# Performance work log

Hardware: AMD Instinct MI355X
Metric: run time of the kernel (lower is better)

## Reference

```python
import jax, jax.numpy as jnp
import numpy as np
import math

RANK = 396

def setup_inputs() -> dict:
    key = jax.random.key(0)
    ks = jax.random.split(key, 8)
    batch, L, wemb, temb, tags, rank = 16, 128, 400, 20, 25, RANK
    std = 0.1545
    return {
        "word_emb": jax.random.normal(ks[0], (batch, L, wemb), dtype=jnp.float32),
        "tag_emd": jax.random.normal(ks[1], (tags, temb), dtype=jnp.float32),
        "W1": jax.random.normal(ks[2], (wemb, rank), dtype=jnp.float32) * std,
        "W2": jax.random.normal(ks[3], (wemb, rank), dtype=jnp.float32) * std,
        "W3": jax.random.normal(ks[4], (wemb, rank), dtype=jnp.float32) * std,
        "T1": jax.random.normal(ks[5], (temb, rank), dtype=jnp.float32) * std,
        "T2": jax.random.normal(ks[6], (temb, rank), dtype=jnp.float32) * std,
        "T3": jax.random.normal(ks[7], (temb, rank), dtype=jnp.float32) * std,
    }

def reference(word_emb, tag_emd, W1, W2, W3, T1, T2, T3):
    # word_emb: [n, L, wemb]; output: [n, L-2, tags, tags, tags]
    g1 = word_emb[:, :-2] @ W1   # [n, m, k]
    g2 = word_emb[:, 1:-1] @ W2
    g3 = word_emb[:, 2:] @ W3
    g4 = tag_emd @ T1            # [a, k]
    g5 = tag_emd @ T2
    g6 = tag_emd @ T3
    temp01 = g1 * g2 * g3                               # [n, m, k]
    temp02 = jnp.einsum('ak,bk,ck->abck', g4, g5, g6)   # [a, b, c, k]
    score = jnp.einsum('nmk,abck->nmabc', temp01, temp02)
    score = score / jnp.asarray(math.sqrt(RANK), score.dtype)
    return score
```

## Files before the change

kernel.cpp:

```cpp
#include <hip/hip_runtime.h>
#include <hip/hip_bf16.h>
#include <stdint.h>

#define KP    416
#define RANKD 396
#define WEMB  400
#define TEMB  20
#define TAGS  25
#define BATCH 16
#define LSEQ  128
#define MROWS 126
#define NM    2016
#define NMP   2048
#define ABC   15625
#define ABCP  15872
#define SCALE 0.050251890762960605f

typedef __attribute__((ext_vector_type(8))) short short8;
typedef __attribute__((ext_vector_type(4))) float f32x4;

#define OFF_T01  0
#define OFF_T02  1703936
#define OFF_WORD 14909440
#define OFF_WT   16613376
#define OFF_G    17651712

#define GLOAD_LDS16(gp, lp) \
  __builtin_amdgcn_global_load_lds((const __attribute__((address_space(1))) uint32_t*)(gp), \
                                   (__attribute__((address_space(3))) uint32_t*)(lp), 16, 0, 0)

__device__ __forceinline__ uint16_t f2bf(float f) {
    union { float f; uint32_t u; } v; v.f = f;
    uint32_t u = v.u;
    return (uint16_t)((u + 0x7FFFu + ((u >> 16) & 1u)) >> 16);
}

#define J1_BLK 3328
#define J2_BLK 2028
#define J3_BLK 122
__global__ void k_prep(const float* __restrict__ word,
                       const float* __restrict__ W1, const float* __restrict__ W2,
                       const float* __restrict__ W3, const float* __restrict__ tag,
                       const float* __restrict__ T1, const float* __restrict__ T2,
                       const float* __restrict__ T3,
                       uint16_t* __restrict__ wordb, uint16_t* __restrict__ wt,
                       float* __restrict__ g) {
    int bx = blockIdx.x;
    if (bx < J1_BLK) {
        int idx = bx * 256 + threadIdx.x;
        int e = idx % KP, row = idx / KP;
        wordb[idx] = f2bf((e < WEMB) ? word[row * WEMB + e] : 0.f);
    } else if (bx < J1_BLK + J2_BLK) {
        int idx = (bx - J1_BLK) * 256 + threadIdx.x;
        int j = idx / (KP * KP);
        int rem = idx % (KP * KP);
        int k = rem / KP, e = rem % KP;
        const float* W = (j == 0) ? W1 : (j == 1) ? W2 : W3;
        wt[idx] = f2bf((k < RANKD && e < WEMB) ? W[e * RANKD + k] : 0.f);
    } else {
        int idx = (bx - J1_BLK - J2_BLK) * 256 + threadIdx.x;
        if (idx >= 3 * TAGS * KP) return;
        int j = idx / (TAGS * KP);
        int rem = idx % (TAGS * KP);
        int a = rem / KP, k = rem % KP;
        const float* T = (j == 0) ? T1 : (j == 1) ? T2 : T3;
        float s = 0.f;
        if (k < RANKD) {
            for (int e = 0; e < TEMB; ++e) s += tag[a * TEMB + e] * T[e * RANKD + k];
        }
        g[idx] = s;
    }
}

#define T01_BLK 896
#define T02_BLK 3224
__global__ __launch_bounds__(256) void k_mid(const uint16_t* __restrict__ word,
                                             const uint16_t* __restrict__ wt,
                                             const float* __restrict__ g,
                                             uint16_t* __restrict__ t01,
                                             uint16_t* __restrict__ t02) {
    int bx = blockIdx.x;
    if (bx < T01_BLK) {
        int wid = threadIdx.x >> 6, lane = threadIdx.x & 63;
        int nmtile = bx & 127;
        int ktile = (bx >> 7) * 4 + wid;
        if (ktile >= KP / 16) return;
        int col_l = lane & 15, kblk = lane >> 4;
        int colk = ktile * 16 + col_l;
        f32x4 acc1 = {0.f, 0.f, 0.f, 0.f}, acc2 = acc1, acc3 = acc1;
        if (nmtile < NM / 16) {
            int nm_a = nmtile * 16 + col_l;
            int n = nm_a / MROWS, m = nm_a % MROWS;
            const uint16_t* arow = word + (size_t)(n * LSEQ + m) * KP;
            const uint16_t* b1 = wt + (size_t)colk * KP;
            const uint16_t* b2 = wt + (size_t)KP * KP + (size_t)colk * KP;
            const uint16_t* b3 = wt + (size_t)2 * KP * KP + (size_t)colk * KP;
            for (int e0 = 0; e0 < KP; e0 += 32) {
                int eo = e0 + kblk * 8;
                short8 a0 = *(const short8*)(arow + eo);
                short8 a1 = *(const short8*)(arow + KP + eo);
                short8 a2 = *(const short8*)(arow + 2 * KP + eo);
                short8 v1 = *(const short8*)(b1 + eo);
                short8 v2 = *(const short8*)(b2 + eo);
                short8 v3 = *(const short8*)(b3 + eo);
                acc1 = __builtin_amdgcn_mfma_f32_16x16x32_bf16(a0, v1, acc1, 0, 0, 0);
                acc2 = __builtin_amdgcn_mfma_f32_16x16x32_bf16(a1, v2, acc2, 0, 0, 0);
                acc3 = __builtin_amdgcn_mfma_f32_16x16x32_bf16(a2, v3, acc3, 0, 0, 0);
            }
        }
        for (int r = 0; r < 4; ++r) {
            int row = nmtile * 16 + kblk * 4 + r;
            float v = acc1[r] * acc2[r] * acc3[r] * SCALE;
            t01[(size_t)row * KP + colk] = f2bf(v);
        }
    } else {
        int idx = (bx - T01_BLK) * 256 + threadIdx.x;
        int abc = idx / (KP / 8), kc = idx % (KP / 8);
        int k0 = kc * 8;
        short8 o;
        if (abc < ABC) {
            int a = abc / 625, rem = abc % 625, b = rem / 25, c = rem % 25;
            const float4* ga = (const float4*)(g + (size_t)a * KP + k0);
            const float4* gb = (const float4*)(g + (size_t)TAGS * KP + (size_t)b * KP + k0);
            const float4* gc = (const float4*)(g + (size_t)2 * TAGS * KP + (size_t)c * KP + k0);
            float4 a0 = ga[0], a1 = ga[1];
            float4 b0 = gb[0], b1 = gb[1];
            float4 c0 = gc[0], c1 = gc[1];
            o[0] = (short)f2bf(a0.x * b0.x * c0.x);
            o[1] = (short)f2bf(a0.y * b0.y * c0.y);
            o[2] = (short)f2bf(a0.z * b0.z * c0.z);
            o[3] = (short)f2bf(a0.w * b0.w * c0.w);
            o[4] = (short)f2bf(a1.x * b1.x * c1.x);
            o[5] = (short)f2bf(a1.y * b1.y * c1.y);
            o[6] = (short)f2bf(a1.z * b1.z * c1.z);
            o[7] = (short)f2bf(a1.w * b1.w * c1.w);
        } else {
            for (int t = 0; t < 8; ++t) o[t] = 0;
        }
        *(short8*)(t02 + (size_t)abc * KP + k0) = o;
    }
}

__global__ __launch_bounds__(256) void k_final(const uint16_t* __restrict__ t01,
                                               const uint16_t* __restrict__ t02,
                                               float* __restrict__ out) {
    __shared__ __align__(16) uint16_t ldsA[64 * KP];
    float* lbuf = (float*)ldsA;

    const int tid = threadIdx.x;
    const int wid = tid >> 6, lane = tid & 63;
    const int col_l = lane & 15, kblk = lane >> 4;

    const int gidx = (blockIdx.x & 7) * 248 + (blockIdx.x >> 3);
    const int mb = gidx & 31, nb = gidx >> 5;
    const int brow = mb * 64, bcol = nb * 256;
    const int wcol = wid * 64;

    {
        const uint16_t* gAsrc = t01 + (size_t)(brow + lane) * KP + wid * 8;
        char* ldst = (char*)ldsA + wid * 1024;
#pragma unroll
        for (int t = 0; t < 13; ++t)
            GLOAD_LDS16(gAsrc + t * 32, ldst + t * 4096);
    }

    const uint16_t* gBn[4];
#pragma unroll
    for (int n = 0; n < 4; ++n)
        gBn[n] = t02 + (size_t)(bcol + wcol + n * 16 + col_l) * KP + kblk * 8;

    f32x4 acc[4][4];
#pragma unroll
    for (int m = 0; m < 4; ++m)
#pragma unroll
        for (int n = 0; n < 4; ++n)
            acc[m][n] = (f32x4){0.f, 0.f, 0.f, 0.f};

    short8 bP[4];
#pragma unroll
    for (int n = 0; n < 4; ++n) bP[n] = *(const short8*)(gBn[n]);

    __syncthreads();

    const int NT = KP / 32;
#pragma unroll
    for (int kt = 0; kt < NT; ++kt) {
        short8 bF[4];
#pragma unroll
        for (int n = 0; n < 4; ++n) bF[n] = bP[n];
        if (kt + 1 < NT) {
#pragma unroll
            for (int n = 0; n < 4; ++n)
                bP[n] = *(const short8*)(gBn[n] + (kt + 1) * 32);
        }
        short8 aF[4];
#pragma unroll
        for (int m = 0; m < 4; ++m)
            aF[m] = *(const short8*)(ldsA + (kt * 4 + kblk) * 512 + (m * 16 + col_l) * 8);
#pragma unroll
        for (int m = 0; m < 4; ++m)
#pragma unroll
            for (int n = 0; n < 4; ++n)
                acc[m][n] = __builtin_amdgcn_mfma_f32_16x16x32_bf16(aF[m], bF[n], acc[m][n], 0, 0, 0);
    }

    __syncthreads();
#pragma unroll
    for (int ch = 0; ch < 2; ++ch) {
#pragma unroll
        for (int mm = 0; mm < 2; ++mm) {
            const int m = ch * 2 + mm;
#pragma unroll
            for (int n = 0; n < 4; ++n)
#pragma unroll
                for (int r = 0; r < 4; ++r) {
                    int row_l = mm * 16 + kblk * 4 + r;
                    int col = wcol + n * 16 + col_l;
                    lbuf[row_l * 260 + col] = acc[m][n][r];
                }
        }
        __syncthreads();
#pragma unroll
        for (int it = 0; it < 8; ++it) {
            int row_l = it * 4 + wid;
            int grow = brow + ch * 32 + row_l;
            int gcol = bcol + lane * 4;
            if (grow < NM) {
                f32x4 v = *(const f32x4*)&lbuf[row_l * 260 + lane * 4];
                float* po = out + (size_t)grow * ABC + gcol;
                if (gcol + 3 < ABC) {
                    __builtin_nontemporal_store(v, (f32x4*)po);
                } else {
                    if (gcol     < ABC) po[0] = v[0];
                    if (gcol + 1 < ABC) po[1] = v[1];
                    if (gcol + 2 < ABC) po[2] = v[2];
                }
            }
        }
        if (ch == 0) __syncthreads();
    }
}

extern "C" void kernel_launch(void* const* d_in, const int* in_sizes, int n_in,
                              void* d_out, int out_size, void* d_ws, size_t ws_size,
                              hipStream_t stream) {
    const float* word = (const float*)d_in[0];
    const float* tag  = (const float*)d_in[1];
    const float* W1   = (const float*)d_in[2];
    const float* W2   = (const float*)d_in[3];
    const float* W3   = (const float*)d_in[4];
    const float* T1   = (const float*)d_in[5];
    const float* T2   = (const float*)d_in[6];
    const float* T3   = (const float*)d_in[7];
    float* out = (float*)d_out;
    char* ws = (char*)d_ws;

    uint16_t* t01   = (uint16_t*)(ws + OFF_T01);
    uint16_t* t02   = (uint16_t*)(ws + OFF_T02);
    uint16_t* wordb = (uint16_t*)(ws + OFF_WORD);
    uint16_t* wt    = (uint16_t*)(ws + OFF_WT);
    float*    g     = (float*)(ws + OFF_G);

    k_prep<<<J1_BLK + J2_BLK + J3_BLK, 256, 0, stream>>>(word, W1, W2, W3, tag,
                                                         T1, T2, T3, wordb, wt, g);
    k_mid<<<T01_BLK + T02_BLK, 256, 0, stream>>>(wordb, wt, g, t01, t02);
    k_final<<<32 * 62, 256, 0, stream>>>(t01, t02, out);
}
```

Before: 82.53 us.

## Retile final GEMM to 32x512 blocks with per-wave 16x256 strips

Changes the output tile of the final bf16 MFMA GEMM from 64x256 to 32x512, so each wave computes a 16-row by 256-column strip with one A fragment from LDS and 16 B fragments streamed from global memory. The 32-row tile matches NM=2016 exactly (63 row blocks), removing the padded rows wasted by the old 64-row tiling, and LDS use shrinks. The XCD-aware block remapping is redone for the new 1953-block grid. In exchange, register pressure grows (16 accumulators and 16 B prefetch registers) and B traffic per output element rises, while the epilogue now needs four LDS staging rounds.

```diff
diff --git a/kernel.cpp b/kernel.cpp
--- a/kernel.cpp
+++ b/kernel.cpp
@@ -144,100 +144,93 @@
 __global__ __launch_bounds__(256) void k_final(const uint16_t* __restrict__ t01,
                                                const uint16_t* __restrict__ t02,
                                                float* __restrict__ out) {
-    __shared__ __align__(16) uint16_t ldsA[64 * KP];
-    float* lbuf = (float*)ldsA;
+    __shared__ __align__(16) char smem[26624];
+    uint16_t* ldsA = (uint16_t*)smem;
+    float* lbuf = (float*)smem;
 
     const int tid = threadIdx.x;
     const int wid = tid >> 6, lane = tid & 63;
     const int col_l = lane & 15, kblk = lane >> 4;
 
-    const int gidx = (blockIdx.x & 7) * 248 + (blockIdx.x >> 3);
-    const int mb = gidx & 31, nb = gidx >> 5;
-    const int brow = mb * 64, bcol = nb * 256;
-    const int wcol = wid * 64;
+    const int xcd = blockIdx.x & 7, bidx = blockIdx.x >> 3;
+    const int wgid = ((xcd == 0) ? 0 : (245 + (xcd - 1) * 244)) + bidx;
+    const int mb = wgid % 63, nb = wgid / 63;
+    const int brow = mb * 32, bcol = nb * 512;
+    const int wrow = (wid >> 1) * 16, wcol = (wid & 1) * 256;
 
     {
-        const uint16_t* gAsrc = t01 + (size_t)(brow + lane) * KP + wid * 8;
-        char* ldst = (char*)ldsA + wid * 1024;
-#pragma unroll
-        for (int t = 0; t < 13; ++t)
-            GLOAD_LDS16(gAsrc + t * 32, ldst + t * 4096);
-    }
-
-    const uint16_t* gBn[4];
-#pragma unroll
-    for (int n = 0; n < 4; ++n)
-        gBn[n] = t02 + (size_t)(bcol + wcol + n * 16 + col_l) * KP + kblk * 8;
-
-    f32x4 acc[4][4];
-#pragma unroll
-    for (int m = 0; m < 4; ++m)
-#pragma unroll
-        for (int n = 0; n < 4; ++n)
-            acc[m][n] = (f32x4){0.f, 0.f, 0.f, 0.f};
-
-    short8 bP[4];
-#pragma unroll
-    for (int n = 0; n < 4; ++n) bP[n] = *(const short8*)(gBn[n]);
+#pragma unroll
+        for (int pass = 0; pass < 6; ++pass) {
+            const uint16_t* src = t01 + (size_t)(brow + (tid & 31)) * KP
+                                  + (pass * 8 + (tid >> 5)) * 8;
+            GLOAD_LDS16(src, smem + pass * 4096 + wid * 1024);
+        }
+        if (tid < 128) {
+            const uint16_t* src = t01 + (size_t)(brow + (tid & 31)) * KP
+                                  + (48 + (tid >> 5)) * 8;
+            GLOAD_LDS16(src, smem + 6 * 4096 + wid * 1024);
+        }
+    }
+
+    const uint16_t* gB = t02 + (size_t)(bcol + wcol + col_l) * KP + kblk * 8;
+
+    f32x4 acc[16];
+#pragma unroll
+    for (int n = 0; n < 16; ++n) acc[n] = (f32x4){0.f, 0.f, 0.f, 0.f};
+
+    short8 bP[16];
+#pragma unroll
+    for (int n = 0; n < 16; ++n)
+        bP[n] = *(const short8*)(gB + (size_t)n * 16 * KP);
 
     __syncthreads();
 
     const int NT = KP / 32;
 #pragma unroll
     for (int kt = 0; kt < NT; ++kt) {
-        short8 bF[4];
-#pragma unroll
-        for (int n = 0; n < 4; ++n) bF[n] = bP[n];
+        short8 bF[16];
+#pragma unroll
+        for (int n = 0; n < 16; ++n) bF[n] = bP[n];
         if (kt + 1 < NT) {
 #pragma unroll
-            for (int n = 0; n < 4; ++n)
-                bP[n] = *(const short8*)(gBn[n] + (kt + 1) * 32);
-        }
-        short8 aF[4];
-#pragma unroll
-        for (int m = 0; m < 4; ++m)
-            aF[m] = *(const short8*)(ldsA + (kt * 4 + kblk) * 512 + (m * 16 + col_l) * 8);
-#pragma unroll
-        for (int m = 0; m < 4; ++m)
-#pragma unroll
-            for (int n = 0; n < 4; ++n)
-                acc[m][n] = __builtin_amdgcn_mfma_f32_16x16x32_bf16(aF[m], bF[n], acc[m][n], 0, 0, 0);
+            for (int n = 0; n < 16; ++n)
+                bP[n] = *(const short8*)(gB + (size_t)n * 16 * KP + (kt + 1) * 32);
+        }
+        short8 aF = *(const short8*)(ldsA + (kt * 4 + kblk) * 256 + (wrow + col_l) * 8);
+#pragma unroll
+        for (int n = 0; n < 16; ++n)
+            acc[n] = __builtin_amdgcn_mfma_f32_16x16x32_bf16(aF, bF[n], acc[n], 0, 0, 0);
     }
 
     __syncthreads();
 #pragma unroll
-    for (int ch = 0; ch < 2; ++ch) {
-#pragma unroll
-        for (int mm = 0; mm < 2; ++mm) {
-            const int m = ch * 2 + mm;
-#pragma unroll
-            for (int n = 0; n < 4; ++n)
-#pragma unroll
-                for (int r = 0; r < 4; ++r) {
-                    int row_l = mm * 16 + kblk * 4 + r;
-                    int col = wcol + n * 16 + col_l;
-                    lbuf[row_l * 260 + col] = acc[m][n][r];
-                }
+    for (int ch = 0; ch < 4; ++ch) {
+        if (((wid >> 1) == (ch >> 1)) && ((kblk >> 1) == (ch & 1))) {
+            int rl0 = (kblk & 1) * 4;
+#pragma unroll
+            for (int n = 0; n < 16; ++n)
+#pragma unroll
+                for (int r = 0; r < 4; ++r)
+                    lbuf[(rl0 + r) * 516 + wcol + n * 16 + col_l] = acc[n][r];
         }
         __syncthreads();
 #pragma unroll
-        for (int it = 0; it < 8; ++it) {
-            int row_l = it * 4 + wid;
-            int grow = brow + ch * 32 + row_l;
-            int gcol = bcol + lane * 4;
-            if (grow < NM) {
-                f32x4 v = *(const f32x4*)&lbuf[row_l * 260 + lane * 4];
-                float* po = out + (size_t)grow * ABC + gcol;
-                if (gcol + 3 < ABC) {
-                    __builtin_nontemporal_store(v, (f32x4*)po);
-                } else {
-                    if (gcol     < ABC) po[0] = v[0];
-                    if (gcol + 1 < ABC) po[1] = v[1];
-                    if (gcol + 2 < ABC) po[2] = v[2];
-                }
+        for (int p = 0; p < 4; ++p) {
+            int gidx = p * 256 + tid;
+            int rl = gidx >> 7, cv = gidx & 127;
+            int grow = brow + ch * 8 + rl;
+            int gcol = bcol + cv * 4;
+            f32x4 v = *(const f32x4*)&lbuf[rl * 516 + cv * 4];
+            float* po = out + (size_t)grow * ABC + gcol;
+            if (gcol + 3 < ABC) {
+                __builtin_nontemporal_store(v, (f32x4*)po);
+            } else {
+                if (gcol     < ABC) po[0] = v[0];
+                if (gcol + 1 < ABC) po[1] = v[1];
+                if (gcol + 2 < ABC) po[2] = v[2];
             }
         }
-        if (ch == 0) __syncthreads();
+        if (ch < 3) __syncthreads();
     }
 }
 
@@ -264,5 +257,5 @@
     k_prep<<<J1_BLK + J2_BLK + J3_BLK, 256, 0, stream>>>(word, W1, W2, W3, tag,
                                                          T1, T2, T3, wordb, wt, g);
     k_mid<<<T01_BLK + T02_BLK, 256, 0, stream>>>(wordb, wt, g, t01, t02);
-    k_final<<<32 * 62, 256, 0, stream>>>(t01, t02, out);
-}
+    k_final<<<63 * 31, 256, 0, stream>>>(t01, t02, out);
+}
```

Measured after the change: 149.6 us. 1.81x slower.

## Process two M tiles per block and prefetch the next A tile during epilogue

Applied to the files above, without the earlier changes.

Each block of the final GEMM now handles two 64-row M tiles, so the grid is halved. The second tile's A panel is loaded into LDS asynchronously while the first tile's results are written out, and the staging buffer for output is now separate from the A panel. Output is staged in 16-row chunks synchronised with explicit lgkmcnt barriers and a partial vmcnt wait. This is meant to overlap the store-heavy epilogue with loading the next operands and to amortise the B fragment setup, at the cost of more LDS per block and fragile hand-written wait counts.

```diff
diff --git a/kernel.cpp b/kernel.cpp
--- a/kernel.cpp
+++ b/kernel.cpp
@@ -33,6 +33,12 @@
     union { float f; uint32_t u; } v; v.f = f;
     uint32_t u = v.u;
     return (uint16_t)((u + 0x7FFFu + ((u >> 16) & 1u)) >> 16);
+}
+
+__device__ __forceinline__ void lgkm_barrier() {
+    asm volatile("s_waitcnt lgkmcnt(0)" ::: "memory");
+    __builtin_amdgcn_s_barrier();
+    __builtin_amdgcn_sched_barrier(0);
 }
 
 #define J1_BLK 3328
@@ -145,17 +151,25 @@
                                                const uint16_t* __restrict__ t02,
                                                float* __restrict__ out) {
     __shared__ __align__(16) uint16_t ldsA[64 * KP];
-    float* lbuf = (float*)ldsA;
+    __shared__ __align__(16) float lbuf[16 * 260];
 
     const int tid = threadIdx.x;
     const int wid = tid >> 6, lane = tid & 63;
     const int col_l = lane & 15, kblk = lane >> 4;
 
-    const int gidx = (blockIdx.x & 7) * 248 + (blockIdx.x >> 3);
-    const int mb = gidx & 31, nb = gidx >> 5;
-    const int brow = mb * 64, bcol = nb * 256;
+    const int gidx = (blockIdx.x & 7) * 124 + (blockIdx.x >> 3);
+    const int mg = gidx & 15, nb = gidx >> 4;
+    const int bcol = nb * 256;
     const int wcol = wid * 64;
 
+    const uint16_t* gBn[4];
+#pragma unroll
+    for (int n = 0; n < 4; ++n)
+        gBn[n] = t02 + (size_t)(bcol + wcol + n * 16 + col_l) * KP + kblk * 8;
+
+    const int NT = KP / 32;
+
+    int brow = mg * 128;
     {
         const uint16_t* gAsrc = t01 + (size_t)(brow + lane) * KP + wid * 8;
         char* ldst = (char*)ldsA + wid * 1024;
@@ -163,81 +177,88 @@
         for (int t = 0; t < 13; ++t)
             GLOAD_LDS16(gAsrc + t * 32, ldst + t * 4096);
     }
-
-    const uint16_t* gBn[4];
-#pragma unroll
-    for (int n = 0; n < 4; ++n)
-        gBn[n] = t02 + (size_t)(bcol + wcol + n * 16 + col_l) * KP + kblk * 8;
-
-    f32x4 acc[4][4];
-#pragma unroll
-    for (int m = 0; m < 4; ++m)
-#pragma unroll
-        for (int n = 0; n < 4; ++n)
-            acc[m][n] = (f32x4){0.f, 0.f, 0.f, 0.f};
-
     short8 bP[4];
 #pragma unroll
     for (int n = 0; n < 4; ++n) bP[n] = *(const short8*)(gBn[n]);
-
     __syncthreads();
 
-    const int NT = KP / 32;
-#pragma unroll
-    for (int kt = 0; kt < NT; ++kt) {
-        short8 bF[4];
-#pragma unroll
-        for (int n = 0; n < 4; ++n) bF[n] = bP[n];
-        if (kt + 1 < NT) {
+#pragma unroll
+    for (int tile = 0; tile < 2; ++tile) {
+        f32x4 acc[4][4];
+#pragma unroll
+        for (int m = 0; m < 4; ++m)
 #pragma unroll
             for (int n = 0; n < 4; ++n)
-                bP[n] = *(const short8*)(gBn[n] + (kt + 1) * 32);
-        }
-        short8 aF[4];
-#pragma unroll
-        for (int m = 0; m < 4; ++m)
-            aF[m] = *(const short8*)(ldsA + (kt * 4 + kblk) * 512 + (m * 16 + col_l) * 8);
-#pragma unroll
-        for (int m = 0; m < 4; ++m)
+                acc[m][n] = (f32x4){0.f, 0.f, 0.f, 0.f};
+
+#pragma unroll
+        for (int kt = 0; kt < NT; ++kt) {
+            short8 bF[4];
+#pragma unroll
+            for (int n = 0; n < 4; ++n) bF[n] = bP[n];
+            if (kt + 1 < NT) {
+#pragma unroll
+                for (int n = 0; n < 4; ++n)
+                    bP[n] = *(const short8*)(gBn[n] + (kt + 1) * 32);
+            }
+            short8 aF[4];
+#pragma unroll
+            for (int m = 0; m < 4; ++m)
+                aF[m] = *(const short8*)(ldsA + (kt * 4 + kblk) * 512 + (m * 16 + col_l) * 8);
+#pragma unroll
+            for (int m = 0; m < 4; ++m)
+#pragma unroll
+                for (int n = 0; n < 4; ++n)
+                    acc[m][n] = __builtin_amdgcn_mfma_f32_16x16x32_bf16(aF[m], bF[n], acc[m][n], 0, 0, 0);
+        }
+
+        lgkm_barrier();
+
+        if (tile == 0) {
+            const uint16_t* gAsrc = t01 + (size_t)(brow + 64 + lane) * KP + wid * 8;
+            char* ldst = (char*)ldsA + wid * 1024;
+#pragma unroll
+            for (int t = 0; t < 13; ++t)
+                GLOAD_LDS16(gAsrc + t * 32, ldst + t * 4096);
+#pragma unroll
+            for (int n = 0; n < 4; ++n) bP[n] = *(const short8*)(gBn[n]);
+        }
+
+#pragma unroll
+        for (int ch = 0; ch < 4; ++ch) {
 #pragma unroll
             for (int n = 0; n < 4; ++n)
-                acc[m][n] = __builtin_amdgcn_mfma_f32_16x16x32_bf16(aF[m], bF[n], acc[m][n], 0, 0, 0);
-    }
-
-    __syncthreads();
-#pragma unroll
-    for (int ch = 0; ch < 2; ++ch) {
-#pragma unroll
-        for (int mm = 0; mm < 2; ++mm) {
-            const int m = ch * 2 + mm;
-#pragma unroll
-            for (int n = 0; n < 4; ++n)
-#pragma unroll
-                for (int r = 0; r < 4; ++r) {
-                    int row_l = mm * 16 + kblk * 4 + r;
-                    int col = wcol + n * 16 + col_l;
-                    lbuf[row_l * 260 + col] = acc[m][n][r];
-                }
-        }
-        __syncthreads();
-#pragma unroll
-        for (int it = 0; it < 8; ++it) {
-            int row_l = it * 4 + wid;
-            int grow = brow + ch * 32 + row_l;
-            int gcol = bcol + lane * 4;
-            if (grow < NM) {
-                f32x4 v = *(const f32x4*)&lbuf[row_l * 260 + lane * 4];
-                float* po = out + (size_t)grow * ABC + gcol;
-                if (gcol + 3 < ABC) {
-                    __builtin_nontemporal_store(v, (f32x4*)po);
-                } else {
-                    if (gcol     < ABC) po[0] = v[0];
-                    if (gcol + 1 < ABC) po[1] = v[1];
-                    if (gcol + 2 < ABC) po[2] = v[2];
+#pragma unroll
+                for (int r = 0; r < 4; ++r)
+                    lbuf[(kblk * 4 + r) * 260 + wcol + n * 16 + col_l] = acc[ch][n][r];
+            lgkm_barrier();
+#pragma unroll
+            for (int p = 0; p < 4; ++p) {
+                int idx = p * 256 + tid;
+                int rl = idx >> 6, cv = idx & 63;
+                int grow = brow + ch * 16 + rl;
+                int gcol = bcol + cv * 4;
+                if (grow < NM) {
+                    f32x4 v = *(const f32x4*)&lbuf[rl * 260 + cv * 4];
+                    float* po = out + (size_t)grow * ABC + gcol;
+                    if (gcol + 3 < ABC) {
+                        __builtin_nontemporal_store(v, (f32x4*)po);
+                    } else {
+                        if (gcol     < ABC) po[0] = v[0];
+                        if (gcol + 1 < ABC) po[1] = v[1];
+                        if (gcol + 2 < ABC) po[2] = v[2];
+                    }
                 }
             }
-        }
-        if (ch == 0) __syncthreads();
+            if (ch < 3) lgkm_barrier();
+        }
+
+        if (tile == 0) {
+            asm volatile("s_waitcnt vmcnt(20)" ::: "memory");
+            __builtin_amdgcn_s_barrier();
+            __builtin_amdgcn_sched_barrier(0);
+            brow += 64;
+        }
     }
 }
 
@@ -264,5 +285,5 @@
     k_prep<<<J1_BLK + J2_BLK + J3_BLK, 256, 0, stream>>>(word, W1, W2, W3, tag,
                                                          T1, T2, T3, wordb, wt, g);
     k_mid<<<T01_BLK + T02_BLK, 256, 0, stream>>>(wordb, wt, g, t01, t02);
-    k_final<<<32 * 62, 256, 0, stream>>>(t01, t02, out);
-}
+    k_final<<<16 * 62, 256, 0, stream>>>(t01, t02, out);
+}
```

Measured after the change: 84.70 us. 1.03x slower.
